# Optimization experiments

Hardware: AMD Instinct MI355X
Metric: run time of the kernel (lower is better)

## Reference

```python
import jax, jax.numpy as jnp
import numpy as np

D = 1024
N_HEAD = 16
D_HEAD = D // N_HEAD
B, S = 4, 2048
EPS = 1e-6


def rmsnorm(x, w):
    # x: [..., d_head]
    return x / jnp.sqrt(jnp.mean(x * x, axis=-1, keepdims=True) + EPS) * w


def setup_inputs() -> dict:
    key = jax.random.key(0)
    ks = jax.random.split(key, 6)
    x = jax.random.normal(ks[0], (B, S, D), dtype=jnp.float32)
    # causal mask: True means masked (upper triangle above diagonal)
    mask = jnp.triu(jnp.ones((S, S), dtype=bool), k=1)
    scale = 1.0 / np.sqrt(D)
    W_qkv = jax.random.normal(ks[1], (D, 3 * D), dtype=jnp.float32) * scale
    b_qkv = jnp.zeros((3 * D,), dtype=jnp.float32)
    W_o = jax.random.normal(ks[2], (D, D), dtype=jnp.float32) * scale
    b_o = jnp.zeros((D,), dtype=jnp.float32)
    wq = jnp.ones((D_HEAD,), dtype=jnp.float32)
    wk = jnp.ones((D_HEAD,), dtype=jnp.float32)
    return {"x": x, "mask": mask, "W_qkv": W_qkv, "b_qkv": b_qkv,
            "W_o": W_o, "b_o": b_o, "wq": wq, "wk": wk}


def reference(x, mask, W_qkv, b_qkv, W_o, b_o, wq, wk):
    b, s, d = x.shape
    qkv = x @ W_qkv + b_qkv  # [b,s,3d]
    q, k, v = jnp.split(qkv, 3, axis=-1)
    q = q.reshape(b, s, N_HEAD, D_HEAD)
    k = k.reshape(b, s, N_HEAD, D_HEAD)
    v = v.reshape(b, s, N_HEAD, D_HEAD)
    q = rmsnorm(q, wq)
    k = rmsnorm(k, wk)
    # NOTE: no 1/sqrt(d_head) scaling, faithful to the source
    attn = jnp.einsum('bqhd,bkhd->bhqk', q, k)
    attn = jnp.where(mask[None, None, :, :], -jnp.inf, attn)
    attn = jax.nn.softmax(attn, axis=-1)
    z = jnp.einsum('bhqk,bkhd->bqhd', attn, v).reshape(b, s, d)
    return z @ W_o + b_o
```

## Files before the change

kernel.cpp:

```cpp
#include <hip/hip_runtime.h>
#include <cmath>

typedef _Float16 half_t;
typedef _Float16 half8 __attribute__((ext_vector_type(8)));
typedef _Float16 half4v __attribute__((ext_vector_type(4)));
typedef float float4v __attribute__((ext_vector_type(4)));

#define LOG2E 1.44269504088896340736f

#define GLDS16(g, l)                                                                   \
    __builtin_amdgcn_global_load_lds((const __attribute__((address_space(1))) void*)(g), \
                                     (__attribute__((address_space(3))) void*)(l), 16, 0, 0)

__global__ void cast_f32_f16(const float* __restrict__ in, half_t* __restrict__ out, int n) {
    int i = (blockIdx.x * blockDim.x + threadIdx.x) * 4;
    if (i >= n) return;
    float4 v = *(const float4*)(in + i);
    half4v o;
    o[0] = (half_t)v.x; o[1] = (half_t)v.y; o[2] = (half_t)v.z; o[3] = (half_t)v.w;
    *(half4v*)(out + i) = o;
}

__global__ void transpose_cast(const float* __restrict__ in, half_t* __restrict__ out, int R, int C) {
    __shared__ float tile[32][33];
    int c0 = blockIdx.x * 32, r0 = blockIdx.y * 32;
    int tx = threadIdx.x, ty = threadIdx.y;
    for (int p = 0; p < 4; p++) {
        int r = r0 + ty + p * 8;
        tile[ty + p * 8][tx] = in[(size_t)r * C + c0 + tx];
    }
    __syncthreads();
    for (int p = 0; p < 4; p++) {
        int c = c0 + ty + p * 8;
        out[(size_t)c * R + r0 + tx] = (half_t)tile[tx][ty + p * 8];
    }
}

template <int MODE>
__global__ __launch_bounds__(256) void gemm_f16(
    const half_t* __restrict__ A,
    const half_t* __restrict__ Bt,
    const float* __restrict__ bias,
    void* __restrict__ Cout,
    int M, int N, int K,
    const float* __restrict__ wq, const float* __restrict__ wk,
    half_t* __restrict__ Qh, half_t* __restrict__ Kh)
{
    __shared__ __align__(16) half_t As[128 * 32];
    __shared__ __align__(16) half_t Bs[128 * 32];
    int t = threadIdx.x;
    int lane = t & 63, w = t >> 6;
    int m0 = blockIdx.x * 128, n0 = blockIdx.y * 128;
    int wm = (w >> 1) * 64, wn = (w & 1) * 64;
    int lrow = lane & 15, quad = lane >> 4;

    int srow = t >> 2, scol = (t & 3) * 8;
    const half_t* gA = A  + (size_t)(m0 + srow) * K + scol;
    const half_t* gB = Bt + (size_t)(n0 + srow) * K + scol;
    half_t* ldsA = As + w * 512;
    half_t* ldsB = Bs + w * 512;

    float4v acc[4][4] = {};

    for (int k0 = 0; k0 < K; k0 += 32) {
        __syncthreads();
        GLDS16(gA + k0,                  ldsA);
        GLDS16(gA + (size_t)64 * K + k0, ldsA + 2048);
        GLDS16(gB + k0,                  ldsB);
        GLDS16(gB + (size_t)64 * K + k0, ldsB + 2048);
        __asm__ volatile("s_waitcnt vmcnt(0)" ::: "memory");
        __syncthreads();
        half8 af[4], bf[4];
        for (int i = 0; i < 4; i++) af[i] = *(const half8*)(&As[(wm + i * 16 + lrow) * 32 + quad * 8]);
        for (int i = 0; i < 4; i++) bf[i] = *(const half8*)(&Bs[(wn + i * 16 + lrow) * 32 + quad * 8]);
        for (int mi = 0; mi < 4; mi++)
            for (int ni = 0; ni < 4; ni++)
                acc[mi][ni] = __builtin_amdgcn_mfma_f32_16x16x32_f16(af[mi], bf[ni], acc[mi][ni], 0, 0, 0);
    }

    if (MODE == 0) {
        float* out = (float*)Cout;
        for (int mi = 0; mi < 4; mi++)
            for (int ni = 0; ni < 4; ni++)
                for (int r = 0; r < 4; r++) {
                    int gr = m0 + wm + mi * 16 + quad * 4 + r;
                    int gc = n0 + wn + ni * 16 + lrow;
                    out[(size_t)gr * N + gc] = acc[mi][ni][r] + bias[gc];
                }
    } else {
        int nglob = n0 + wn;
        if (nglob < 2048) {
            int isK = nglob >> 10;
            int h = (nglob >> 6) & 15;
            const float* wv = isK ? wk : wq;
            half_t* dst = isK ? Kh : Qh;
            for (int mi = 0; mi < 4; mi++)
                for (int r = 0; r < 4; r++) {
                    int gr = m0 + wm + mi * 16 + quad * 4 + r;
                    float v[4]; float ss = 0.f;
                    for (int ni = 0; ni < 4; ni++) {
                        v[ni] = acc[mi][ni][r] + bias[nglob + ni * 16 + lrow];
                        ss += v[ni] * v[ni];
                    }
                    ss += __shfl_xor(ss, 1);
                    ss += __shfl_xor(ss, 2);
                    ss += __shfl_xor(ss, 4);
                    ss += __shfl_xor(ss, 8);
                    float rr = rsqrtf(ss * (1.0f / 64.0f) + 1e-6f);
                    int bb = gr >> 11, s = gr & 2047;
                    size_t rowbase = ((size_t)((bb * 16 + h) * 2048 + s)) * 64;
                    for (int ni = 0; ni < 4; ni++) {
                        int d = ni * 16 + lrow;
                        dst[rowbase + d] = (half_t)(v[ni] * rr * wv[d]);
                    }
                }
        } else {
            half_t* qv = (half_t*)Cout;
            for (int mi = 0; mi < 4; mi++)
                for (int ni = 0; ni < 4; ni++)
                    for (int r = 0; r < 4; r++) {
                        int gr = m0 + wm + mi * 16 + quad * 4 + r;
                        int gc = nglob + ni * 16 + lrow;
                        qv[(size_t)gr * 1024 + (gc - 2048)] = (half_t)(acc[mi][ni][r] + bias[gc]);
                    }
        }
    }
}

__global__ void v_transpose(const half_t* __restrict__ qv, half_t* __restrict__ Vt) {
    __shared__ half_t tile[32][40];
    int s0 = blockIdx.x * 32;
    int d0 = blockIdx.y * 32;
    int bh = blockIdx.z;
    int b = bh >> 4, h = bh & 15;
    int tx = threadIdx.x, ty = threadIdx.y;
    for (int p = 0; p < 4; p++) {
        int s = s0 + ty + p * 8;
        tile[ty + p * 8][tx] = qv[((size_t)(b * 2048 + s)) * 1024 + h * 64 + d0 + tx];
    }
    __syncthreads();
    for (int p = 0; p < 4; p++) {
        int d = d0 + ty + p * 8;
        Vt[((size_t)bh * 64 + d) * 2048 + s0 + tx] = tile[tx][ty + p * 8];
    }
}

__global__ __launch_bounds__(512, 4) void attn(
    const half_t* __restrict__ Qh, const half_t* __restrict__ Kh, const half_t* __restrict__ Vt,
    half_t* __restrict__ Z)
{
    __shared__ __align__(16) half_t Ks[2][64 * 64];
    __shared__ __align__(16) half_t Vs[2][64 * 64];
    __shared__ __align__(16) half_t Ps[8 * 16 * 64];

    int bh = blockIdx.x;
    int b = bh >> 4, h = bh & 15;
    int t = threadIdx.x, lane = t & 63, w = t >> 6;
    int lrow = lane & 15, quad = lane >> 4;

    int sr = w * 8 + (lane >> 3);
    int scc = (lane & 7) ^ ((lane >> 3) & 7);
    const half_t* gK0 = Kh + ((size_t)bh * 2048 + sr) * 64 + scc * 8;
    const half_t* gV0 = Vt + ((size_t)bh * 64 + sr) * 2048 + scc * 8;

    int sw = lrow & 7;
    int cA = (quad ^ sw) * 8;
    int cB = ((quad + 4) ^ sw) * 8;
    half_t* PsW = Ps + w * 1024 + lrow * 64;

    for (int pass = 0; pass < 2; pass++) {
        int qt = pass ? (15 - (int)blockIdx.y) : (int)blockIdx.y;
        int q0w = qt * 128 + w * 16;

        const half_t* Qbase = Qh + ((size_t)bh * 2048 + q0w + lrow) * 64;
        half8 qf0 = *(const half8*)(Qbase + quad * 8);
        half8 qf1 = *(const half8*)(Qbase + 32 + quad * 8);

        float4v ot[4] = {};
        float m = -__builtin_inff(), l = 0.f;

        int nt = 2 * qt + 2;
        __syncthreads();
        GLDS16(gK0, &Ks[0][w * 512]);
        GLDS16(gV0, &Vs[0][w * 512]);

        for (int kt = 0; kt < nt; kt++) {
            int cur = kt & 1, nxt = cur ^ 1;
            int kb = kt * 64;
            __syncthreads();
            if (kt + 1 < nt) {
                GLDS16(gK0 + (size_t)(kb + 64) * 64, &Ks[nxt][w * 512]);
                GLDS16(gV0 + kb + 64,                &Vs[nxt][w * 512]);
                __asm__ volatile("s_waitcnt vmcnt(2)" ::: "memory");
            } else {
                __asm__ volatile("s_waitcnt vmcnt(0)" ::: "memory");
            }
            __syncthreads();
            if (kb > q0w + 15) continue;

            float4v st[4];
            for (int f = 0; f < 4; f++) {
                float4v z = {};
                const half_t* kr = &Ks[cur][(f * 16 + lrow) * 64];
                half8 k0 = *(const half8*)(kr + cA);
                half8 k1 = *(const half8*)(kr + cB);
                z = __builtin_amdgcn_mfma_f32_16x16x32_f16(k0, qf0, z, 0, 0, 0);
                z = __builtin_amdgcn_mfma_f32_16x16x32_f16(k1, qf1, z, 0, 0, 0);
                st[f] = z;
            }
            if (kb + 63 > q0w) {
                int qabs = q0w + lrow;
                for (int f = 0; f < 4; f++)
                    for (int r = 0; r < 4; r++) {
                        int key = kb + f * 16 + quad * 4 + r;
                        if (key > qabs) st[f][r] = -__builtin_inff();
                    }
            }
            float tm = st[0][0];
            for (int f = 0; f < 4; f++)
                for (int r = 0; r < 4; r++) tm = fmaxf(tm, st[f][r]);
            tm = fmaxf(tm, __shfl_xor(tm, 16));
            tm = fmaxf(tm, __shfl_xor(tm, 32));
            float mn = fmaxf(m, tm);
            float alpha = exp2f((m - mn) * LOG2E);
            m = mn;
            float rs = 0.f;
            for (int f = 0; f < 4; f++) {
                half4v ph;
                for (int r = 0; r < 4; r++) {
                    float p = exp2f((st[f][r] - mn) * LOG2E);
                    rs += p;
                    ph[r] = (half_t)p;
                }
                int cc = (2 * f + (quad >> 1)) ^ sw;
                *(half4v*)(PsW + cc * 8 + (quad & 1) * 4) = ph;
            }
            rs += __shfl_xor(rs, 16);
            rs += __shfl_xor(rs, 32);
            l = l * alpha + rs;
            for (int f2 = 0; f2 < 4; f2++)
                for (int r = 0; r < 4; r++) ot[f2][r] *= alpha;

            __asm__ volatile("s_waitcnt lgkmcnt(0)" ::: "memory");
            half8 p0 = *(const half8*)(PsW + cA);
            half8 p1 = *(const half8*)(PsW + cB);
            for (int f2 = 0; f2 < 4; f2++) {
                const half_t* vr = &Vs[cur][(f2 * 16 + lrow) * 64];
                half8 v0 = *(const half8*)(vr + cA);
                half8 v1 = *(const half8*)(vr + cB);
                ot[f2] = __builtin_amdgcn_mfma_f32_16x16x32_f16(v0, p0, ot[f2], 0, 0, 0);
                ot[f2] = __builtin_amdgcn_mfma_f32_16x16x32_f16(v1, p1, ot[f2], 0, 0, 0);
            }
        }

        float inv = 1.0f / l;
        size_t base = ((size_t)(b * 2048) + q0w + lrow) * 1024 + h * 64;
        for (int f2 = 0; f2 < 4; f2++) {
            half4v oh;
            for (int r = 0; r < 4; r++) oh[r] = (half_t)(ot[f2][r] * inv);
            *(half4v*)(Z + base + f2 * 16 + quad * 4) = oh;
        }
    }
}

extern "C" void kernel_launch(void* const* d_in, const int* in_sizes, int n_in,
                              void* d_out, int out_size, void* d_ws, size_t ws_size,
                              hipStream_t stream)
{
    const float* x     = (const float*)d_in[0];
    const float* W_qkv = (const float*)d_in[2];
    const float* b_qkv = (const float*)d_in[3];
    const float* W_o   = (const float*)d_in[4];
    const float* b_o   = (const float*)d_in[5];
    const float* wq    = (const float*)d_in[6];
    const float* wk    = (const float*)d_in[7];
    float* out = (float*)d_out;

    char* ws = (char*)d_ws;
    half_t* xh   = (half_t*)(ws);
    half_t* Wqt  = (half_t*)(ws + (16ull << 20));
    half_t* Wot  = (half_t*)(ws + (22ull << 20));
    half_t* qkvV = (half_t*)(ws + (24ull << 20));
    half_t* Qh   = (half_t*)(ws + (40ull << 20));
    half_t* Kh   = (half_t*)(ws + (56ull << 20));
    half_t* Vt   = (half_t*)(ws + (72ull << 20));
    half_t* zh   = xh;

    cast_f32_f16<<<8192, 256, 0, stream>>>(x, xh, 8192 * 1024);
    transpose_cast<<<dim3(96, 32), dim3(32, 8), 0, stream>>>(W_qkv, Wqt, 1024, 3072);
    transpose_cast<<<dim3(32, 32), dim3(32, 8), 0, stream>>>(W_o, Wot, 1024, 1024);
    gemm_f16<1><<<dim3(64, 24), 256, 0, stream>>>(xh, Wqt, b_qkv, qkvV, 8192, 3072, 1024,
                                                  wq, wk, Qh, Kh);
    v_transpose<<<dim3(64, 2, 64), dim3(32, 8), 0, stream>>>(qkvV, Vt);
    attn<<<dim3(64, 8), 512, 0, stream>>>(Qh, Kh, Vt, zh);
    gemm_f16<0><<<dim3(64, 8), 256, 0, stream>>>(zh, Wot, b_o, out, 8192, 1024, 1024,
                                                 nullptr, nullptr, nullptr, nullptr);
}
```

Measured before the change: 313.3 us.

## Double-buffer GEMM LDS loads and write V transposed directly from QKV GEMM

The GEMM main loop now uses two LDS buffers and issues the global-to-LDS loads for the next K tile before computing the current one, waiting only on the older loads. This is meant to overlap memory latency with MFMA work. Separately, the QKV GEMM epilogue writes the V slice straight into the transposed [b,h,d,s] layout with 4-wide half stores, which removes the v_transpose kernel and its intermediate buffer round trip. The cost is double the LDS footprint per block, which may reduce occupancy, and strided V stores along s.

```diff
diff --git a/kernel.cpp b/kernel.cpp
--- a/kernel.cpp
+++ b/kernel.cpp
@@ -46,8 +46,8 @@
     const float* __restrict__ wq, const float* __restrict__ wk,
     half_t* __restrict__ Qh, half_t* __restrict__ Kh)
 {
-    __shared__ __align__(16) half_t As[128 * 32];
-    __shared__ __align__(16) half_t Bs[128 * 32];
+    __shared__ __align__(16) half_t As[2][128 * 32];
+    __shared__ __align__(16) half_t Bs[2][128 * 32];
     int t = threadIdx.x;
     int lane = t & 63, w = t >> 6;
     int m0 = blockIdx.x * 128, n0 = blockIdx.y * 128;
@@ -57,22 +57,32 @@
     int srow = t >> 2, scol = (t & 3) * 8;
     const half_t* gA = A  + (size_t)(m0 + srow) * K + scol;
     const half_t* gB = Bt + (size_t)(n0 + srow) * K + scol;
-    half_t* ldsA = As + w * 512;
-    half_t* ldsB = Bs + w * 512;
+    half_t* ldsA[2] = { &As[0][w * 512], &As[1][w * 512] };
+    half_t* ldsB[2] = { &Bs[0][w * 512], &Bs[1][w * 512] };
 
     float4v acc[4][4] = {};
 
+    GLDS16(gA,                  ldsA[0]);
+    GLDS16(gA + (size_t)64 * K, ldsA[0] + 2048);
+    GLDS16(gB,                  ldsB[0]);
+    GLDS16(gB + (size_t)64 * K, ldsB[0] + 2048);
+
     for (int k0 = 0; k0 < K; k0 += 32) {
+        int cur = (k0 >> 5) & 1, nxt = cur ^ 1;
         __syncthreads();
-        GLDS16(gA + k0,                  ldsA);
-        GLDS16(gA + (size_t)64 * K + k0, ldsA + 2048);
-        GLDS16(gB + k0,                  ldsB);
-        GLDS16(gB + (size_t)64 * K + k0, ldsB + 2048);
-        __asm__ volatile("s_waitcnt vmcnt(0)" ::: "memory");
+        if (k0 + 32 < K) {
+            GLDS16(gA + k0 + 32,                  ldsA[nxt]);
+            GLDS16(gA + (size_t)64 * K + k0 + 32, ldsA[nxt] + 2048);
+            GLDS16(gB + k0 + 32,                  ldsB[nxt]);
+            GLDS16(gB + (size_t)64 * K + k0 + 32, ldsB[nxt] + 2048);
+            __asm__ volatile("s_waitcnt vmcnt(4)" ::: "memory");
+        } else {
+            __asm__ volatile("s_waitcnt vmcnt(0)" ::: "memory");
+        }
         __syncthreads();
         half8 af[4], bf[4];
-        for (int i = 0; i < 4; i++) af[i] = *(const half8*)(&As[(wm + i * 16 + lrow) * 32 + quad * 8]);
-        for (int i = 0; i < 4; i++) bf[i] = *(const half8*)(&Bs[(wn + i * 16 + lrow) * 32 + quad * 8]);
+        for (int i = 0; i < 4; i++) af[i] = *(const half8*)(&As[cur][(wm + i * 16 + lrow) * 32 + quad * 8]);
+        for (int i = 0; i < 4; i++) bf[i] = *(const half8*)(&Bs[cur][(wn + i * 16 + lrow) * 32 + quad * 8]);
         for (int mi = 0; mi < 4; mi++)
             for (int ni = 0; ni < 4; ni++)
                 acc[mi][ni] = __builtin_amdgcn_mfma_f32_16x16x32_f16(af[mi], bf[ni], acc[mi][ni], 0, 0, 0);
@@ -115,33 +125,19 @@
                     }
                 }
         } else {
-            half_t* qv = (half_t*)Cout;
-            for (int mi = 0; mi < 4; mi++)
-                for (int ni = 0; ni < 4; ni++)
-                    for (int r = 0; r < 4; r++) {
-                        int gr = m0 + wm + mi * 16 + quad * 4 + r;
-                        int gc = nglob + ni * 16 + lrow;
-                        qv[(size_t)gr * 1024 + (gc - 2048)] = (half_t)(acc[mi][ni][r] + bias[gc]);
-                    }
-        }
-    }
-}
-
-__global__ void v_transpose(const half_t* __restrict__ qv, half_t* __restrict__ Vt) {
-    __shared__ half_t tile[32][40];
-    int s0 = blockIdx.x * 32;
-    int d0 = blockIdx.y * 32;
-    int bh = blockIdx.z;
-    int b = bh >> 4, h = bh & 15;
-    int tx = threadIdx.x, ty = threadIdx.y;
-    for (int p = 0; p < 4; p++) {
-        int s = s0 + ty + p * 8;
-        tile[ty + p * 8][tx] = qv[((size_t)(b * 2048 + s)) * 1024 + h * 64 + d0 + tx];
-    }
-    __syncthreads();
-    for (int p = 0; p < 4; p++) {
-        int d = d0 + ty + p * 8;
-        Vt[((size_t)bh * 64 + d) * 2048 + s0 + tx] = tile[tx][ty + p * 8];
+            half_t* Vt = (half_t*)Cout;
+            for (int mi = 0; mi < 4; mi++) {
+                int gr = m0 + wm + mi * 16 + quad * 4;
+                int bb = gr >> 11, s = gr & 2047;
+                for (int ni = 0; ni < 4; ni++) {
+                    int dg = nglob + ni * 16 + lrow - 2048;
+                    float bv = bias[nglob + ni * 16 + lrow];
+                    half4v oh;
+                    for (int r = 0; r < 4; r++) oh[r] = (half_t)(acc[mi][ni][r] + bv);
+                    *(half4v*)(Vt + ((size_t)((bb * 16 + (dg >> 6)) * 64 + (dg & 63))) * 2048 + s) = oh;
+                }
+            }
+        }
     }
 }
 
@@ -280,7 +276,6 @@
     half_t* xh   = (half_t*)(ws);
     half_t* Wqt  = (half_t*)(ws + (16ull << 20));
     half_t* Wot  = (half_t*)(ws + (22ull << 20));
-    half_t* qkvV = (half_t*)(ws + (24ull << 20));
     half_t* Qh   = (half_t*)(ws + (40ull << 20));
     half_t* Kh   = (half_t*)(ws + (56ull << 20));
     half_t* Vt   = (half_t*)(ws + (72ull << 20));
@@ -289,9 +284,8 @@
     cast_f32_f16<<<8192, 256, 0, stream>>>(x, xh, 8192 * 1024);
     transpose_cast<<<dim3(96, 32), dim3(32, 8), 0, stream>>>(W_qkv, Wqt, 1024, 3072);
     transpose_cast<<<dim3(32, 32), dim3(32, 8), 0, stream>>>(W_o, Wot, 1024, 1024);
-    gemm_f16<1><<<dim3(64, 24), 256, 0, stream>>>(xh, Wqt, b_qkv, qkvV, 8192, 3072, 1024,
+    gemm_f16<1><<<dim3(64, 24), 256, 0, stream>>>(xh, Wqt, b_qkv, Vt, 8192, 3072, 1024,
                                                   wq, wk, Qh, Kh);
-    v_transpose<<<dim3(64, 2, 64), dim3(32, 8), 0, stream>>>(qkvV, Vt);
     attn<<<dim3(64, 8), 512, 0, stream>>>(Qh, Kh, Vt, zh);
     gemm_f16<0><<<dim3(64, 8), 256, 0, stream>>>(zh, Wot, b_o, out, 8192, 1024, 1024,
                                                  nullptr, nullptr, nullptr, nullptr);
```

New measurement: 306.1 us. -2.3%, faster.
